# Kernel tuning notes

Hardware: AMD Instinct MI355X
Metric: run time of the kernel (lower is better)

Reference implementation:

```python
import jax, jax.numpy as jnp
import numpy as np
import math

DIM = 1536; NH = 12; HD = 128
F, H, W = 6, 30, 30
S = F * H * W
B = 1
K_LEN = 9900  # hardcoded k_lens in the source forward
EPS_NORM = 1e-6


def _rope_tables(max_len=1024, d=HD):
    # Wan rope_params: three tables of widths d-4*(d//6), 2*(d//6), 2*(d//6)
    # -> cos/sin tables of half-widths 22, 21, 21 (concat = d//2 = 64)
    def ang(dd):
        inv = 1.0 / (10000.0 ** (np.arange(0, dd, 2, dtype=np.float64) / dd))
        return np.outer(np.arange(max_len, dtype=np.float64), inv)
    a = np.concatenate([ang(d - 4 * (d // 6)), ang(2 * (d // 6)), ang(2 * (d // 6))], axis=1)
    return np.cos(a).astype(np.float32), np.sin(a).astype(np.float32)


def setup_inputs() -> dict:
    key = jax.random.key(0)
    ks = jax.random.split(key, 5)
    s = 1.0 / math.sqrt(DIM)
    cos, sin = _rope_tables()
    return {
        "x": jax.random.normal(ks[0], (B, S, DIM), jnp.float32),
        "q_w": jax.random.normal(ks[1], (DIM, DIM), jnp.float32) * s,
        "q_b": jnp.zeros((DIM,), jnp.float32),
        "k_w": jax.random.normal(ks[2], (DIM, DIM), jnp.float32) * s,
        "k_b": jnp.zeros((DIM,), jnp.float32),
        "v_w": jax.random.normal(ks[3], (DIM, DIM), jnp.float32) * s,
        "v_b": jnp.zeros((DIM,), jnp.float32),
        "o_w": jax.random.normal(ks[4], (DIM, DIM), jnp.float32) * s,
        "o_b": jnp.zeros((DIM,), jnp.float32),
        "norm_q_w": jnp.ones((DIM,), jnp.float32),
        "norm_k_w": jnp.ones((DIM,), jnp.float32),
        "freqs_cos": jnp.asarray(cos),
        "freqs_sin": jnp.asarray(sin),
        "grid_f": F, "grid_h": H, "grid_w": W,
    }


def rms_norm(x, w):
    # RMSNorm over full model dim, computed in fp32 (as in source)
    xf = x.astype(jnp.float32)
    xn = xf * jax.lax.rsqrt(jnp.mean(xf * xf, axis=-1, keepdims=True) + EPS_NORM)
    return xn.astype(x.dtype) * w


def rope_apply(x, cos, sin, f, h, w):
    # x: [B,S,N,D]; rotate consecutive pairs with 3D-factorized (f,h,w) freqs
    Bb, Ss, Nn, Dd = x.shape
    c = Dd // 2
    sp = [c - 2 * (c // 3), c // 3, c // 3]  # 22, 21, 21

    def grid(tab):
        tf = tab[:, :sp[0]]
        th = tab[:, sp[0]:sp[0] + sp[1]]
        tw = tab[:, sp[0] + sp[1]:]
        g = jnp.concatenate([
            jnp.broadcast_to(tf[:f, None, None, :], (f, h, w, sp[0])),
            jnp.broadcast_to(th[None, :h, None, :], (f, h, w, sp[1])),
            jnp.broadcast_to(tw[None, None, :w, :], (f, h, w, sp[2])),
        ], axis=-1)
        return g.reshape(f * h * w, 1, c)  # [S,1,c] (broadcast over heads)

    gc, gs = grid(cos), grid(sin)
    xp = x.astype(jnp.float32).reshape(Bb, Ss, Nn, c, 2)
    xr, xi = xp[..., 0], xp[..., 1]
    orr = xr * gc - xi * gs
    oii = xr * gs + xi * gc
    return jnp.stack([orr, oii], axis=-1).reshape(Bb, Ss, Nn, Dd).astype(x.dtype)


def attention(q, k, v, k_len):
    # full attention (window_size=(-1,-1)) with keys masked beyond k_len
    scale = 1.0 / math.sqrt(q.shape[-1])
    att = jnp.einsum('bqnd,bknd->bnqk', q, k) * scale
    valid = jnp.arange(k.shape[1]) < k_len
    att = jnp.where(valid[None, None, None, :], att, jnp.finfo(att.dtype).min)
    p = jax.nn.softmax(att, axis=-1)
    return jnp.einsum('bnqk,bknd->bqnd', p, v)


def reference(x, q_w, q_b, k_w, k_b, v_w, v_b, o_w, o_b, norm_q_w, norm_k_w, freqs_cos, freqs_sin, grid_f, grid_h, grid_w):
    Bb, Ss, _ = x.shape
    q = rms_norm(x @ q_w.T + q_b, norm_q_w).reshape(Bb, Ss, NH, HD)
    k = rms_norm(x @ k_w.T + k_b, norm_k_w).reshape(Bb, Ss, NH, HD)
    v = (x @ v_w.T + v_b).reshape(Bb, Ss, NH, HD)
    q = rope_apply(q, freqs_cos, freqs_sin, grid_f, grid_h, grid_w)
    k = rope_apply(k, freqs_cos, freqs_sin, grid_f, grid_h, grid_w)
    o = attention(q, k, v, K_LEN).reshape(Bb, Ss, NH * HD)
    return o @ o_w.T + o_b
```

## Files before the change

### kernel.cpp

```cpp
#include <hip/hip_runtime.h>

#define DIM 1536
#define NH 12
#define HD 128
#define S_LEN 5400
#define SPAD 5440
#define MPAD 5504
#define NQKV 4608
#define EPS_NORM 1e-6f

typedef __bf16 bf16_t;
typedef __bf16 bf16x8 __attribute__((ext_vector_type(8)));
typedef __bf16 bf16x4 __attribute__((ext_vector_type(4)));
typedef __bf16 bf16x2 __attribute__((ext_vector_type(2)));
typedef float  f32x4  __attribute__((ext_vector_type(4)));
typedef float  f32x16 __attribute__((ext_vector_type(16)));
typedef int    i32x2  __attribute__((ext_vector_type(2)));

#define GLOAD_LDS16(gp, lp) __builtin_amdgcn_global_load_lds( \
    (__attribute__((address_space(1))) void*)(void*)(gp),     \
    (__attribute__((address_space(3))) void*)(lp), 16, 0, 0)

__device__ __forceinline__ unsigned int pkbf(float a, float b) {
  union { bf16x2 h; unsigned int u; } c;
  c.h[0] = (__bf16)a; c.h[1] = (__bf16)b;
  return c.u;
}

__device__ __forceinline__ float xhalf_max(float x) {
  i32x2 r = __builtin_amdgcn_permlane32_swap(__float_as_int(x), __float_as_int(x),
                                             false, false);
  return fmaxf(__int_as_float(r.x), __int_as_float(r.y));
}
__device__ __forceinline__ float xhalf_sum(float x) {
  i32x2 r = __builtin_amdgcn_permlane32_swap(__float_as_int(x), __float_as_int(x),
                                             false, false);
  return __int_as_float(r.x) + __int_as_float(r.y);
}


__global__ __launch_bounds__(256) void cvt_x_kernel(const float* __restrict__ x,
                                                    bf16_t* __restrict__ xb) {
  size_t base = ((size_t)blockIdx.x * 256 + threadIdx.x) * 4;
  if (base >= (size_t)MPAD * DIM) return;
  size_t row = base / DIM;
  float4 v = make_float4(0.f, 0.f, 0.f, 0.f);
  if (row < S_LEN) v = *(const float4*)&x[base];
  bf16x4 o; o[0] = (__bf16)v.x; o[1] = (__bf16)v.y; o[2] = (__bf16)v.z; o[3] = (__bf16)v.w;
  *(bf16x4*)&xb[base] = o;
}

__global__ __launch_bounds__(256) void cvt_wqkv_kernel(const float* __restrict__ qw,
                                                       const float* __restrict__ kw,
                                                       const float* __restrict__ vw,
                                                       bf16_t* __restrict__ wb) {
  size_t base = ((size_t)blockIdx.x * 256 + threadIdx.x) * 4;
  if (base >= (size_t)NQKV * DIM) return;
  int row = (int)(base / DIM);
  int col = (int)(base - (size_t)row * DIM);
  const float* src; int rr = row;
  if (rr >= 3072)      { src = vw; rr -= 3072; }
  else if (rr >= 1536) { src = kw; rr -= 1536; }
  else                 { src = qw; }
  float4 v = *(const float4*)&src[(size_t)rr * DIM + col];
  bf16x4 o; o[0] = (__bf16)v.x; o[1] = (__bf16)v.y; o[2] = (__bf16)v.z; o[3] = (__bf16)v.w;
  *(bf16x4*)&wb[base] = o;
}

__global__ __launch_bounds__(256) void cvt_wo_kernel(const float* __restrict__ w,
                                                     bf16_t* __restrict__ wb) {
  size_t base = ((size_t)blockIdx.x * 256 + threadIdx.x) * 4;
  if (base >= (size_t)DIM * DIM) return;
  float4 v = *(const float4*)&w[base];
  bf16x4 o; o[0] = (__bf16)v.x; o[1] = (__bf16)v.y; o[2] = (__bf16)v.z; o[3] = (__bf16)v.w;
  *(bf16x4*)&wb[base] = o;
}


template<bool OUT_BF16>
__global__ __launch_bounds__(256) void gemm_bt_kernel(
    const bf16_t* __restrict__ A, const bf16_t* __restrict__ B, void* __restrict__ C,
    const float* __restrict__ bias0, const float* __restrict__ bias1,
    const float* __restrict__ bias2, int M, int N, int K, int Mvalid) {
  __shared__ bf16_t As[2][128 * 32];
  __shared__ bf16_t Bs[2][128 * 32];
  int tid = threadIdx.x;
  int lane = tid & 63, wave = tid >> 6, quad = lane >> 4, l16 = lane & 15;
  int m0 = blockIdx.y * 128, n0 = blockIdx.x * 128;
  int wm = (wave >> 1) * 64, wn = (wave & 1) * 64;
  const bf16_t* Ab = A + (size_t)m0 * K;
  const bf16_t* Bb = B + (size_t)n0 * K;
  f32x4 acc[4][4] = {};

  int eo0 = tid * 8;
  int row0 = eo0 >> 5, col0 = eo0 & 31;
  int eo1 = (256 + tid) * 8;
  int row1 = eo1 >> 5, col1 = eo1 & 31;

  GLOAD_LDS16(Ab + (size_t)row0 * K + col0, &As[0][eo0]);
  GLOAD_LDS16(Bb + (size_t)row0 * K + col0, &Bs[0][eo0]);
  GLOAD_LDS16(Ab + (size_t)row1 * K + col1, &As[0][eo1]);
  GLOAD_LDS16(Bb + (size_t)row1 * K + col1, &Bs[0][eo1]);
  asm volatile("s_waitcnt vmcnt(0)" ::: "memory");
  __builtin_amdgcn_s_barrier();
  __builtin_amdgcn_sched_barrier(0);

  int KT = K >> 5;
  for (int t = 0; t < KT; t++) {
    int cur = t & 1;
    if (t + 1 < KT) {
      int kn = (t + 1) << 5;
      GLOAD_LDS16(Ab + (size_t)row0 * K + kn + col0, &As[cur ^ 1][eo0]);
      GLOAD_LDS16(Bb + (size_t)row0 * K + kn + col0, &Bs[cur ^ 1][eo0]);
      GLOAD_LDS16(Ab + (size_t)row1 * K + kn + col1, &As[cur ^ 1][eo1]);
      GLOAD_LDS16(Bb + (size_t)row1 * K + kn + col1, &Bs[cur ^ 1][eo1]);
    }
    bf16x8 af[4], bfr[4];
#pragma unroll
    for (int i = 0; i < 4; i++)
      af[i] = *(const bf16x8*)&As[cur][(wm + i * 16 + l16) * 32 + quad * 8];
#pragma unroll
    for (int j = 0; j < 4; j++)
      bfr[j] = *(const bf16x8*)&Bs[cur][(wn + j * 16 + l16) * 32 + quad * 8];
#pragma unroll
    for (int i = 0; i < 4; i++)
#pragma unroll
      for (int j = 0; j < 4; j++)
        acc[i][j] = __builtin_amdgcn_mfma_f32_16x16x32_bf16(af[i], bfr[j], acc[i][j], 0, 0, 0);
    asm volatile("s_waitcnt vmcnt(0) lgkmcnt(0)" ::: "memory");
    __builtin_amdgcn_s_barrier();
    __builtin_amdgcn_sched_barrier(0);
  }
#pragma unroll
  for (int j = 0; j < 4; j++) {
    int n = n0 + wn + j * 16 + l16;
    float bias = (n < 1536) ? bias0[n] : (n < 3072) ? bias1[n - 1536] : bias2[n - 3072];
#pragma unroll
    for (int i = 0; i < 4; i++) {
#pragma unroll
      for (int r = 0; r < 4; r++) {
        int m = m0 + wm + i * 16 + quad * 4 + r;
        float v = acc[i][j][r] + bias;
        if (OUT_BF16) {
          ((bf16_t*)C)[(size_t)m * N + n] = (__bf16)v;
        } else {
          if (m < Mvalid) ((float*)C)[(size_t)m * N + n] = v;
        }
      }
    }
  }
}


__global__ __launch_bounds__(256) void rope_qk_kernel(
    const bf16_t* __restrict__ qkv, const float* __restrict__ nqw,
    const float* __restrict__ nkw, const float* __restrict__ fcos,
    const float* __restrict__ fsin, bf16_t* __restrict__ qout,
    bf16_t* __restrict__ kout) {
  int s = blockIdx.x;
  int tid = threadIdx.x;
  bool valid = s < S_LEN;
  int f = s / 900, hh = (s / 30) % 30, ww = s % 30;
  __shared__ float red[4];
  for (int which = 0; which < 2; which++) {
    const bf16_t* src = qkv + (size_t)s * NQKV + which * DIM;
    const float* nw = which ? nkw : nqw;
    bf16_t* dst = (which ? kout : qout) + (size_t)s * DIM;
    float osc = which ? 1.0f : 0.12751742686f;
    float v[6]; float ss = 0.f;
#pragma unroll
    for (int i = 0; i < 6; i++) {
      v[i] = valid ? (float)src[tid * 6 + i] : 0.f;
      ss += v[i] * v[i];
    }
#pragma unroll
    for (int off = 32; off >= 1; off >>= 1) ss += __shfl_down(ss, off);
    if ((tid & 63) == 0) red[tid >> 6] = ss;
    __syncthreads();
    float tot = red[0] + red[1] + red[2] + red[3];
    float rn = rsqrtf(tot * (1.f / DIM) + EPS_NORM);
    __syncthreads();
#pragma unroll
    for (int i = 0; i < 3; i++) {
      int e0 = tid * 6 + 2 * i;
      int p = e0 >> 1;
      int cc = p & 63;
      int pos = (cc < 22) ? f : (cc < 43) ? hh : ww;
      float c = fcos[pos * 64 + cc], sn = fsin[pos * 64 + cc];
      float xr = v[2 * i] * rn * nw[e0];
      float xi = v[2 * i + 1] * rn * nw[e0 + 1];
      dst[e0]     = (__bf16)((xr * c - xi * sn) * osc);
      dst[e0 + 1] = (__bf16)((xr * sn + xi * c) * osc);
    }
  }
}


__global__ __launch_bounds__(256) void v_transpose_kernel(const bf16_t* __restrict__ qkv,
                                                          bf16_t* __restrict__ vt) {
  __shared__ bf16_t tile[64][136];
  int h = blockIdx.y, s0 = blockIdx.x * 64, tid = threadIdx.x;
#pragma unroll
  for (int it = 0; it < 4; it++) {
    int eo = (it * 256 + tid) * 8;
    int row = eo >> 7, col = eo & 127;
    int s = s0 + row;
    bf16x8 val = {};
    if (s < S_LEN) val = *(const bf16x8*)&qkv[(size_t)s * NQKV + 3072 + h * HD + col];
    *(bf16x8*)&tile[row][col] = val;
  }
  __syncthreads();
  int d = tid & 127, j0 = (tid >> 7) * 32;
  bf16x8 outv[4];
#pragma unroll
  for (int b = 0; b < 4; b++)
#pragma unroll
    for (int j = 0; j < 8; j++) outv[b][j] = tile[j0 + b * 8 + j][d];
  size_t base = ((size_t)h * HD + d) * SPAD + s0 + j0;
#pragma unroll
  for (int b = 0; b < 4; b++) *(bf16x8*)&vt[base + b * 8] = outv[b];
}


__global__ __launch_bounds__(256, 2) void flash_attn_kernel(
    const bf16_t* __restrict__ q, const bf16_t* __restrict__ k,
    const bf16_t* __restrict__ vt, bf16_t* __restrict__ o) {
  __shared__ bf16_t Ks[2][64 * 128];
  __shared__ bf16_t Vs[2][64 * 128];
  int head = blockIdx.y;
  int s0 = blockIdx.x * 128;
  int tid = threadIdx.x, w = tid >> 6, lane = tid & 63;
  int l31 = lane & 31, hh = lane >> 5;

  bf16x8 bq[8];
  {
    const bf16_t* qp = &q[(size_t)(s0 + w * 32 + l31) * DIM + head * HD + hh * 8];
#pragma unroll
    for (int kc = 0; kc < 8; kc++) bq[kc] = *(const bf16x8*)(qp + kc * 16);
  }

  float m_i = -1e30f, l_i = 0.f;
  f32x16 oacc[4] = {};

  const int NT = SPAD / 64;

#pragma unroll
  for (int it = 0; it < 4; it++) {
    int slot = it * 256 + tid;
    int row = slot >> 4, pc = slot & 15;
    int c = pc ^ (row & 15);
    GLOAD_LDS16(k + (size_t)row * DIM + head * HD + c * 8, &Ks[0][slot * 8]);
  }
#pragma unroll
  for (int it = 0; it < 4; it++) {
    int slot = it * 256 + tid;
    int row = slot >> 4, pc = slot & 15;
    int cp = pc ^ (row & 15);
    int d = 2 * row + (cp >> 3);
    GLOAD_LDS16(vt + ((size_t)head * HD + d) * SPAD + (cp & 7) * 8, &Vs[0][slot * 8]);
  }
  asm volatile("s_waitcnt vmcnt(0)" ::: "memory");
  __builtin_amdgcn_s_barrier();
  __builtin_amdgcn_sched_barrier(0);

  for (int t = 0; t < NT; t++) {
    int kt = t * 64;
    int cur = t & 1;

    if (t + 1 < NT) {
      int kn = kt + 64;
#pragma unroll
      for (int it = 0; it < 4; it++) {
        int slot = it * 256 + tid;
        int row = slot >> 4, pc = slot & 15;
        int c = pc ^ (row & 15);
        GLOAD_LDS16(k + (size_t)(kn + row) * DIM + head * HD + c * 8, &Ks[cur ^ 1][slot * 8]);
      }
#pragma unroll
      for (int it = 0; it < 4; it++) {
        int slot = it * 256 + tid;
        int row = slot >> 4, pc = slot & 15;
        int cp = pc ^ (row & 15);
        int d = 2 * row + (cp >> 3);
        GLOAD_LDS16(vt + ((size_t)head * HD + d) * SPAD + kn + (cp & 7) * 8, &Vs[cur ^ 1][slot * 8]);
      }
    }

    f32x16 sacc[2] = {};
    __builtin_amdgcn_s_setprio(1);
#pragma unroll
    for (int ns = 0; ns < 2; ns++) {
      int row = ns * 32 + l31;
#pragma unroll
      for (int kc = 0; kc < 8; kc++) {
        int pc = (kc * 2 + hh) ^ (row & 15);
        bf16x8 ak = *(const bf16x8*)&Ks[cur][row * 128 + pc * 8];
        sacc[ns] = __builtin_amdgcn_mfma_f32_32x32x16_bf16(ak, bq[kc], sacc[ns], 0, 0, 0);
      }
    }
    __builtin_amdgcn_s_setprio(0);

    if (kt + 64 > S_LEN) {
#pragma unroll
      for (int ns = 0; ns < 2; ns++)
#pragma unroll
        for (int r = 0; r < 16; r++) {
          int kvg = kt + ns * 32 + (r & 3) + 8 * (r >> 2) + 4 * hh;
          if (kvg >= S_LEN) sacc[ns][r] = -1e30f;
        }
    }

    float mx;
    {
      float tm[8];
#pragma unroll
      for (int i = 0; i < 8; i++)
        tm[i] = fmaxf(fmaxf(sacc[0][i], sacc[0][i + 8]),
                      fmaxf(sacc[1][i], sacc[1][i + 8]));
#pragma unroll
      for (int i = 0; i < 4; i++) tm[i] = fmaxf(tm[i], tm[i + 4]);
      mx = fmaxf(fmaxf(tm[0], tm[2]), fmaxf(tm[1], tm[3]));
    }
    mx = xhalf_max(mx);
    if (!__all(mx - m_i <= 11.5f)) {
      float mn = fmaxf(m_i, mx);
      float al = __builtin_amdgcn_exp2f(m_i - mn);
      l_i *= al;
#pragma unroll
      for (int dt = 0; dt < 4; dt++)
#pragma unroll
        for (int r = 0; r < 16; r++) oacc[dt][r] *= al;
      m_i = mn;
    }
#pragma unroll
    for (int ns = 0; ns < 2; ns++)
#pragma unroll
      for (int r = 0; r < 16; r++)
        sacc[ns][r] = __builtin_amdgcn_exp2f(sacc[ns][r] - m_i);
    float rs;
    {
      float ts[8];
#pragma unroll
      for (int i = 0; i < 8; i++)
        ts[i] = (sacc[0][i] + sacc[0][i + 8]) + (sacc[1][i] + sacc[1][i + 8]);
#pragma unroll
      for (int i = 0; i < 4; i++) ts[i] += ts[i + 4];
      rs = (ts[0] + ts[2]) + (ts[1] + ts[3]);
    }
    l_i += xhalf_sum(rs);

    __builtin_amdgcn_s_setprio(1);
#pragma unroll
    for (int kvc = 0; kvc < 4; kvc++) {
      int ns = kvc >> 1, rb = (kvc & 1) * 8;
      int w0 = (int)pkbf(sacc[ns][rb + 0], sacc[ns][rb + 1]);
      int w1 = (int)pkbf(sacc[ns][rb + 2], sacc[ns][rb + 3]);
      int w2 = (int)pkbf(sacc[ns][rb + 4], sacc[ns][rb + 5]);
      int w3 = (int)pkbf(sacc[ns][rb + 6], sacc[ns][rb + 7]);
      i32x2 r02 = __builtin_amdgcn_permlane32_swap(w0, w2, false, false);
      i32x2 r13 = __builtin_amdgcn_permlane32_swap(w1, w3, false, false);
      union { unsigned int u[4]; bf16x8 v8; } bpu;
      bpu.u[0] = (unsigned int)r02.x; bpu.u[1] = (unsigned int)r13.x;
      bpu.u[2] = (unsigned int)r02.y; bpu.u[3] = (unsigned int)r13.y;
      bf16x8 bp = bpu.v8;
#pragma unroll
      for (int dt = 0; dt < 4; dt++) {
        int d = dt * 32 + l31;
        int r = d >> 1;
        int cp = ((d & 1) << 3) | (kvc * 2 + hh);
        int pc = cp ^ (r & 15);
        bf16x8 av = *(const bf16x8*)&Vs[cur][r * 128 + pc * 8];
        oacc[dt] = __builtin_amdgcn_mfma_f32_32x32x16_bf16(av, bp, oacc[dt], 0, 0, 0);
      }
    }
    __builtin_amdgcn_s_setprio(0);

    asm volatile("s_waitcnt vmcnt(0) lgkmcnt(0)" ::: "memory");
    __builtin_amdgcn_s_barrier();
    __builtin_amdgcn_sched_barrier(0);
  }

  bf16_t* scr = ((bf16_t*)Ks) + w * (32 * 64);
  float inv = 1.f / l_i;
  int qr = lane >> 1, seg = lane & 1;
  int srow = s0 + w * 32 + qr;
#pragma unroll
  for (int half = 0; half < 2; half++) {
#pragma unroll
    for (int dl = 0; dl < 2; dl++) {
      int dt = half * 2 + dl;
#pragma unroll
      for (int tt = 0; tt < 4; tt++) {
        bf16x4 v;
#pragma unroll
        for (int r4 = 0; r4 < 4; r4++) v[r4] = (__bf16)(oacc[dt][tt * 4 + r4] * inv);
        int c8 = dl * 8 + 2 * tt + hh;
        int pc8 = c8 ^ (l31 & 15);
        *(bf16x4*)&scr[l31 * 64 + pc8 * 4] = v;
      }
    }
#pragma unroll
    for (int i = 0; i < 4; i++) {
      int c8 = seg * 8 + 2 * i;
      bf16x4 lo = *(const bf16x4*)&scr[qr * 64 + ((c8) ^ (qr & 15)) * 4];
      bf16x4 hi = *(const bf16x4*)&scr[qr * 64 + ((c8 + 1) ^ (qr & 15)) * 4];
      bf16x8 val;
#pragma unroll
      for (int j = 0; j < 4; j++) { val[j] = lo[j]; val[j + 4] = hi[j]; }
      if (srow < S_LEN)
        *(bf16x8*)&o[(size_t)srow * DIM + head * HD + half * 64 + seg * 32 + i * 8] = val;
    }
  }
}


extern "C" void kernel_launch(void* const* d_in, const int* in_sizes, int n_in,
                              void* d_out, int out_size, void* d_ws, size_t ws_size,
                              hipStream_t stream) {
  const float* x    = (const float*)d_in[0];
  const float* q_w  = (const float*)d_in[1];
  const float* q_b  = (const float*)d_in[2];
  const float* k_w  = (const float*)d_in[3];
  const float* k_b  = (const float*)d_in[4];
  const float* v_w  = (const float*)d_in[5];
  const float* v_b  = (const float*)d_in[6];
  const float* o_w  = (const float*)d_in[7];
  const float* o_b  = (const float*)d_in[8];
  const float* nqw  = (const float*)d_in[9];
  const float* nkw  = (const float*)d_in[10];
  const float* fcos = (const float*)d_in[11];
  const float* fsin = (const float*)d_in[12];

  char* ws = (char*)d_ws;
  bf16_t* xb   = (bf16_t*)(ws + 0);
  bf16_t* wqkv = (bf16_t*)(ws + 16908288);
  bf16_t* wob  = (bf16_t*)(ws + 31064064);
  bf16_t* qkv  = (bf16_t*)(ws + 35782656);
  bf16_t* qb   = (bf16_t*)(ws + 86507520);
  bf16_t* kb   = (bf16_t*)(ws + 103415808);
  bf16_t* vtb  = (bf16_t*)(ws + 0);
  bf16_t* aob  = (bf16_t*)(ws + 35782656);

  cvt_x_kernel<<<(MPAD * DIM / 4 + 255) / 256, 256, 0, stream>>>(x, xb);
  cvt_wqkv_kernel<<<(NQKV * DIM / 4 + 255) / 256, 256, 0, stream>>>(q_w, k_w, v_w, wqkv);
  cvt_wo_kernel<<<(DIM * DIM / 4 + 255) / 256, 256, 0, stream>>>(o_w, wob);

  gemm_bt_kernel<true><<<dim3(NQKV / 128, MPAD / 128), 256, 0, stream>>>(
      xb, wqkv, qkv, q_b, k_b, v_b, MPAD, NQKV, DIM, MPAD);

  rope_qk_kernel<<<MPAD, 256, 0, stream>>>(qkv, nqw, nkw, fcos, fsin, qb, kb);
  v_transpose_kernel<<<dim3(SPAD / 64, NH), 256, 0, stream>>>(qkv, vtb);

  flash_attn_kernel<<<dim3(MPAD / 128, NH), 256, 0, stream>>>(qb, kb, vtb, aob);

  gemm_bt_kernel<false><<<dim3(DIM / 128, MPAD / 128), 256, 0, stream>>>(
      aob, wob, d_out, o_b, o_b, o_b, MPAD, DIM, DIM, S_LEN);
}
```

Before: 657.5 us.

## Split flash attention over two KV halves with a combine kernel

Splits the key/value sequence into two halves along a new grid dimension, so the attention launch has twice as many blocks. Each half writes unnormalized fp32 partial outputs plus running max and sum, and a new combine kernel merges them into the bf16 attention output. The double-buffered LDS prefetch is replaced by single-buffered synchronous loads, which halves LDS use and allows four blocks per CU. The cost is a load wait on every tile with no overlap, extra fp32 global traffic for the partials, and one more kernel launch.

```diff
diff --git a/kernel.cpp b/kernel.cpp
--- a/kernel.cpp
+++ b/kernel.cpp
@@ -222,12 +222,15 @@
 }
 
 
-__global__ __launch_bounds__(256, 2) void flash_attn_kernel(
+__global__ __launch_bounds__(256, 4) void flash_attn_kernel(
     const bf16_t* __restrict__ q, const bf16_t* __restrict__ k,
-    const bf16_t* __restrict__ vt, bf16_t* __restrict__ o) {
-  __shared__ bf16_t Ks[2][64 * 128];
-  __shared__ bf16_t Vs[2][64 * 128];
+    const bf16_t* __restrict__ vt, float* __restrict__ op0,
+    float* __restrict__ op1, float* __restrict__ mlp) {
+  __shared__ __align__(16) char lds_raw[32768];
+  bf16_t* Ks = (bf16_t*)lds_raw;
+  bf16_t* Vs = (bf16_t*)(lds_raw + 16384);
   int head = blockIdx.y;
+  int kvh = blockIdx.z;
   int s0 = blockIdx.x * 128;
   int tid = threadIdx.x, w = tid >> 6, lane = tid & 63;
   int l31 = lane & 31, hh = lane >> 5;
@@ -242,49 +245,30 @@
   float m_i = -1e30f, l_i = 0.f;
   f32x16 oacc[4] = {};
 
-  const int NT = SPAD / 64;
-
-#pragma unroll
-  for (int it = 0; it < 4; it++) {
-    int slot = it * 256 + tid;
-    int row = slot >> 4, pc = slot & 15;
-    int c = pc ^ (row & 15);
-    GLOAD_LDS16(k + (size_t)row * DIM + head * HD + c * 8, &Ks[0][slot * 8]);
-  }
-#pragma unroll
-  for (int it = 0; it < 4; it++) {
-    int slot = it * 256 + tid;
-    int row = slot >> 4, pc = slot & 15;
-    int cp = pc ^ (row & 15);
-    int d = 2 * row + (cp >> 3);
-    GLOAD_LDS16(vt + ((size_t)head * HD + d) * SPAD + (cp & 7) * 8, &Vs[0][slot * 8]);
-  }
-  asm volatile("s_waitcnt vmcnt(0)" ::: "memory");
-  __builtin_amdgcn_s_barrier();
-  __builtin_amdgcn_sched_barrier(0);
-
-  for (int t = 0; t < NT; t++) {
+  int tstart = kvh ? 43 : 0;
+  int tend   = kvh ? 85 : 43;
+
+  for (int t = tstart; t < tend; t++) {
     int kt = t * 64;
-    int cur = t & 1;
-
-    if (t + 1 < NT) {
-      int kn = kt + 64;
-#pragma unroll
-      for (int it = 0; it < 4; it++) {
-        int slot = it * 256 + tid;
-        int row = slot >> 4, pc = slot & 15;
-        int c = pc ^ (row & 15);
-        GLOAD_LDS16(k + (size_t)(kn + row) * DIM + head * HD + c * 8, &Ks[cur ^ 1][slot * 8]);
-      }
-#pragma unroll
-      for (int it = 0; it < 4; it++) {
-        int slot = it * 256 + tid;
-        int row = slot >> 4, pc = slot & 15;
-        int cp = pc ^ (row & 15);
-        int d = 2 * row + (cp >> 3);
-        GLOAD_LDS16(vt + ((size_t)head * HD + d) * SPAD + kn + (cp & 7) * 8, &Vs[cur ^ 1][slot * 8]);
-      }
-    }
+
+#pragma unroll
+    for (int it = 0; it < 4; it++) {
+      int slot = it * 256 + tid;
+      int row = slot >> 4, pc = slot & 15;
+      int c = pc ^ (row & 15);
+      GLOAD_LDS16(k + (size_t)(kt + row) * DIM + head * HD + c * 8, &Ks[slot * 8]);
+    }
+#pragma unroll
+    for (int it = 0; it < 4; it++) {
+      int slot = it * 256 + tid;
+      int row = slot >> 4, pc = slot & 15;
+      int cp = pc ^ (row & 15);
+      int d = 2 * row + (cp >> 3);
+      GLOAD_LDS16(vt + ((size_t)head * HD + d) * SPAD + kt + (cp & 7) * 8, &Vs[slot * 8]);
+    }
+    asm volatile("s_waitcnt vmcnt(0)" ::: "memory");
+    __builtin_amdgcn_s_barrier();
+    __builtin_amdgcn_sched_barrier(0);
 
     f32x16 sacc[2] = {};
     __builtin_amdgcn_s_setprio(1);
@@ -294,7 +278,7 @@
 #pragma unroll
       for (int kc = 0; kc < 8; kc++) {
         int pc = (kc * 2 + hh) ^ (row & 15);
-        bf16x8 ak = *(const bf16x8*)&Ks[cur][row * 128 + pc * 8];
+        bf16x8 ak = *(const bf16x8*)&Ks[row * 128 + pc * 8];
         sacc[ns] = __builtin_amdgcn_mfma_f32_32x32x16_bf16(ak, bq[kc], sacc[ns], 0, 0, 0);
       }
     }
@@ -369,48 +353,75 @@
         int r = d >> 1;
         int cp = ((d & 1) << 3) | (kvc * 2 + hh);
         int pc = cp ^ (r & 15);
-        bf16x8 av = *(const bf16x8*)&Vs[cur][r * 128 + pc * 8];
+        bf16x8 av = *(const bf16x8*)&Vs[r * 128 + pc * 8];
         oacc[dt] = __builtin_amdgcn_mfma_f32_32x32x16_bf16(av, bp, oacc[dt], 0, 0, 0);
       }
     }
     __builtin_amdgcn_s_setprio(0);
 
-    asm volatile("s_waitcnt vmcnt(0) lgkmcnt(0)" ::: "memory");
+    asm volatile("s_waitcnt lgkmcnt(0)" ::: "memory");
     __builtin_amdgcn_s_barrier();
     __builtin_amdgcn_sched_barrier(0);
   }
 
-  bf16_t* scr = ((bf16_t*)Ks) + w * (32 * 64);
-  float inv = 1.f / l_i;
+  float* scrf = (float*)(lds_raw + (size_t)w * 8192);
+  float* op = kvh ? op1 : op0;
   int qr = lane >> 1, seg = lane & 1;
   int srow = s0 + w * 32 + qr;
 #pragma unroll
-  for (int half = 0; half < 2; half++) {
+  for (int dhalf = 0; dhalf < 2; dhalf++) {
 #pragma unroll
     for (int dl = 0; dl < 2; dl++) {
-      int dt = half * 2 + dl;
+      int dt = dhalf * 2 + dl;
 #pragma unroll
       for (int tt = 0; tt < 4; tt++) {
-        bf16x4 v;
-#pragma unroll
-        for (int r4 = 0; r4 < 4; r4++) v[r4] = (__bf16)(oacc[dt][tt * 4 + r4] * inv);
+        f32x4 v;
+#pragma unroll
+        for (int r4 = 0; r4 < 4; r4++) v[r4] = oacc[dt][tt * 4 + r4];
         int c8 = dl * 8 + 2 * tt + hh;
         int pc8 = c8 ^ (l31 & 15);
-        *(bf16x4*)&scr[l31 * 64 + pc8 * 4] = v;
+        *(f32x4*)&scrf[l31 * 64 + pc8 * 4] = v;
       }
     }
 #pragma unroll
     for (int i = 0; i < 4; i++) {
       int c8 = seg * 8 + 2 * i;
-      bf16x4 lo = *(const bf16x4*)&scr[qr * 64 + ((c8) ^ (qr & 15)) * 4];
-      bf16x4 hi = *(const bf16x4*)&scr[qr * 64 + ((c8 + 1) ^ (qr & 15)) * 4];
-      bf16x8 val;
-#pragma unroll
-      for (int j = 0; j < 4; j++) { val[j] = lo[j]; val[j + 4] = hi[j]; }
-      if (srow < S_LEN)
-        *(bf16x8*)&o[(size_t)srow * DIM + head * HD + half * 64 + seg * 32 + i * 8] = val;
-    }
-  }
+      f32x4 lo = *(const f32x4*)&scrf[qr * 64 + ((c8) ^ (qr & 15)) * 4];
+      f32x4 hi = *(const f32x4*)&scrf[qr * 64 + ((c8 + 1) ^ (qr & 15)) * 4];
+      size_t ob = ((size_t)srow * NH + head) * HD + dhalf * 64 + seg * 32 + i * 8;
+      *(f32x4*)&op[ob] = lo;
+      *(f32x4*)&op[ob + 4] = hi;
+    }
+  }
+  if (hh == 0) {
+    int qg = s0 + w * 32 + l31;
+    *(float2*)&mlp[(((size_t)kvh * NH + head) * MPAD + qg) * 2] = make_float2(m_i, l_i);
+  }
+}
+
+
+__global__ __launch_bounds__(256) void combine_kernel(
+    const float* __restrict__ op0, const float* __restrict__ op1,
+    const float* __restrict__ mlp, bf16_t* __restrict__ aob) {
+  size_t idx = (size_t)blockIdx.x * 256 + threadIdx.x;
+  if (idx >= (size_t)MPAD * NH * 32) return;
+  int dc = (int)(idx & 31);
+  int head = (int)((idx >> 5) % NH);
+  int s = (int)(idx / (NH * 32));
+  float2 a0 = *(const float2*)&mlp[(((size_t)0 * NH + head) * MPAD + s) * 2];
+  float2 a1 = *(const float2*)&mlp[(((size_t)1 * NH + head) * MPAD + s) * 2];
+  float m = fmaxf(a0.x, a1.x);
+  float w0 = __builtin_amdgcn_exp2f(a0.x - m);
+  float w1 = __builtin_amdgcn_exp2f(a1.x - m);
+  float inv = 1.f / (a0.y * w0 + a1.y * w1);
+  w0 *= inv; w1 *= inv;
+  size_t ob = ((size_t)s * NH + head) * HD + (size_t)dc * 4;
+  f32x4 x0 = *(const f32x4*)&op0[ob];
+  f32x4 x1 = *(const f32x4*)&op1[ob];
+  bf16x4 o4;
+#pragma unroll
+  for (int j = 0; j < 4; j++) o4[j] = (__bf16)(x0[j] * w0 + x1[j] * w1);
+  *(bf16x4*)&aob[ob] = o4;
 }
 
 
@@ -439,7 +450,10 @@
   bf16_t* qb   = (bf16_t*)(ws + 86507520);
   bf16_t* kb   = (bf16_t*)(ws + 103415808);
   bf16_t* vtb  = (bf16_t*)(ws + 0);
-  bf16_t* aob  = (bf16_t*)(ws + 35782656);
+  float*  op0p = (float*)(ws + 35782656);
+  float*  op1p = (float*)(ws + 120324096);
+  float*  mlpp = (float*)(ws + 154140672);
+  bf16_t* aob  = (bf16_t*)(ws + 103415808);
 
   cvt_x_kernel<<<(MPAD * DIM / 4 + 255) / 256, 256, 0, stream>>>(x, xb);
   cvt_wqkv_kernel<<<(NQKV * DIM / 4 + 255) / 256, 256, 0, stream>>>(q_w, k_w, v_w, wqkv);
@@ -451,7 +465,11 @@
   rope_qk_kernel<<<MPAD, 256, 0, stream>>>(qkv, nqw, nkw, fcos, fsin, qb, kb);
   v_transpose_kernel<<<dim3(SPAD / 64, NH), 256, 0, stream>>>(qkv, vtb);
 
-  flash_attn_kernel<<<dim3(MPAD / 128, NH), 256, 0, stream>>>(qb, kb, vtb, aob);
+  flash_attn_kernel<<<dim3(MPAD / 128, NH, 2), 256, 0, stream>>>(
+      qb, kb, vtb, op0p, op1p, mlpp);
+
+  combine_kernel<<<(MPAD * NH * 32 + 255) / 256, 256, 0, stream>>>(
+      op0p, op1p, mlpp, aob);
 
   gemm_bt_kernel<false><<<dim3(DIM / 128, MPAD / 128), 256, 0, stream>>>(
       aob, wob, d_out, o_b, o_b, o_b, MPAD, DIM, DIM, S_LEN);
```

Result: slower. 1.074 ms (+63.4%).

## Use 128-key tiles without double buffering and XCD-aware block remap in flash attention

Applied to the files above, without the earlier changes.

The flash attention kernel now processes 128 keys per iteration instead of 64, halving the number of barriers and softmax rescale steps per query block. The K/V double buffer is dropped: each iteration loads the full tile, waits, then computes, so global loads no longer overlap with MFMA work. A 1D grid with an XCD-aware remap groups blocks of the same head onto one XCD to improve L2 reuse of K/V. SPAD grows to 5504 so the padded length divides by 128, which adds some masked padding work and loses load/compute overlap.

```diff
diff --git a/kernel.cpp b/kernel.cpp
--- a/kernel.cpp
+++ b/kernel.cpp
@@ -4,7 +4,7 @@
 #define NH 12
 #define HD 128
 #define S_LEN 5400
-#define SPAD 5440
+#define SPAD 5504
 #define MPAD 5504
 #define NQKV 4608
 #define EPS_NORM 1e-6f
@@ -225,10 +225,17 @@
 __global__ __launch_bounds__(256, 2) void flash_attn_kernel(
     const bf16_t* __restrict__ q, const bf16_t* __restrict__ k,
     const bf16_t* __restrict__ vt, bf16_t* __restrict__ o) {
-  __shared__ bf16_t Ks[2][64 * 128];
-  __shared__ bf16_t Vs[2][64 * 128];
-  int head = blockIdx.y;
-  int s0 = blockIdx.x * 128;
+  __shared__ __align__(16) char lds_raw[65536];
+  bf16_t* Ks = (bf16_t*)lds_raw;
+  bf16_t* Vs = (bf16_t*)(lds_raw + 32768);
+  int nwg = gridDim.x;
+  int bid = blockIdx.x;
+  int xcd = bid & 7, idx = bid >> 3;
+  int q8 = nwg >> 3, rr = nwg & 7;
+  int work = (xcd < rr ? xcd * (q8 + 1) : rr * (q8 + 1) + (xcd - rr) * q8) + idx;
+  int head = work / 43;
+  int s0 = (work - head * 43) * 128;
+
   int tid = threadIdx.x, w = tid >> 6, lane = tid & 63;
   int l31 = lane & 31, hh = lane >> 5;
 
@@ -242,67 +249,50 @@
   float m_i = -1e30f, l_i = 0.f;
   f32x16 oacc[4] = {};
 
-  const int NT = SPAD / 64;
-
-#pragma unroll
-  for (int it = 0; it < 4; it++) {
-    int slot = it * 256 + tid;
-    int row = slot >> 4, pc = slot & 15;
-    int c = pc ^ (row & 15);
-    GLOAD_LDS16(k + (size_t)row * DIM + head * HD + c * 8, &Ks[0][slot * 8]);
-  }
-#pragma unroll
-  for (int it = 0; it < 4; it++) {
-    int slot = it * 256 + tid;
-    int row = slot >> 4, pc = slot & 15;
-    int cp = pc ^ (row & 15);
-    int d = 2 * row + (cp >> 3);
-    GLOAD_LDS16(vt + ((size_t)head * HD + d) * SPAD + (cp & 7) * 8, &Vs[0][slot * 8]);
-  }
-  asm volatile("s_waitcnt vmcnt(0)" ::: "memory");
-  __builtin_amdgcn_s_barrier();
-  __builtin_amdgcn_sched_barrier(0);
+  const int NT = SPAD / 128;
 
   for (int t = 0; t < NT; t++) {
-    int kt = t * 64;
-    int cur = t & 1;
-
-    if (t + 1 < NT) {
-      int kn = kt + 64;
-#pragma unroll
-      for (int it = 0; it < 4; it++) {
-        int slot = it * 256 + tid;
-        int row = slot >> 4, pc = slot & 15;
-        int c = pc ^ (row & 15);
-        GLOAD_LDS16(k + (size_t)(kn + row) * DIM + head * HD + c * 8, &Ks[cur ^ 1][slot * 8]);
-      }
+    int kt = t * 128;
+
+#pragma unroll
+    for (int it = 0; it < 8; it++) {
+      int slot = it * 256 + tid;
+      int row = slot >> 4, pc = slot & 15;
+      int c = pc ^ (row & 15);
+      GLOAD_LDS16(k + (size_t)(kt + row) * DIM + head * HD + c * 8, &Ks[slot * 8]);
+    }
+#pragma unroll
+    for (int h2 = 0; h2 < 2; h2++)
 #pragma unroll
       for (int it = 0; it < 4; it++) {
         int slot = it * 256 + tid;
         int row = slot >> 4, pc = slot & 15;
         int cp = pc ^ (row & 15);
         int d = 2 * row + (cp >> 3);
-        GLOAD_LDS16(vt + ((size_t)head * HD + d) * SPAD + kn + (cp & 7) * 8, &Vs[cur ^ 1][slot * 8]);
-      }
-    }
-
-    f32x16 sacc[2] = {};
+        GLOAD_LDS16(vt + ((size_t)head * HD + d) * SPAD + kt + h2 * 64 + (cp & 7) * 8,
+                    &Vs[h2 * 8192 + slot * 8]);
+      }
+    asm volatile("s_waitcnt vmcnt(0)" ::: "memory");
+    __builtin_amdgcn_s_barrier();
+    __builtin_amdgcn_sched_barrier(0);
+
+    f32x16 sacc[4] = {};
     __builtin_amdgcn_s_setprio(1);
 #pragma unroll
-    for (int ns = 0; ns < 2; ns++) {
+    for (int ns = 0; ns < 4; ns++) {
       int row = ns * 32 + l31;
 #pragma unroll
       for (int kc = 0; kc < 8; kc++) {
         int pc = (kc * 2 + hh) ^ (row & 15);
-        bf16x8 ak = *(const bf16x8*)&Ks[cur][row * 128 + pc * 8];
+        bf16x8 ak = *(const bf16x8*)&Ks[row * 128 + pc * 8];
         sacc[ns] = __builtin_amdgcn_mfma_f32_32x32x16_bf16(ak, bq[kc], sacc[ns], 0, 0, 0);
       }
     }
     __builtin_amdgcn_s_setprio(0);
 
-    if (kt + 64 > S_LEN) {
-#pragma unroll
-      for (int ns = 0; ns < 2; ns++)
+    if (kt + 128 > S_LEN) {
+#pragma unroll
+      for (int ns = 0; ns < 4; ns++)
 #pragma unroll
         for (int r = 0; r < 16; r++) {
           int kvg = kt + ns * 32 + (r & 3) + 8 * (r >> 2) + 4 * hh;
@@ -314,9 +304,13 @@
     {
       float tm[8];
 #pragma unroll
-      for (int i = 0; i < 8; i++)
-        tm[i] = fmaxf(fmaxf(sacc[0][i], sacc[0][i + 8]),
-                      fmaxf(sacc[1][i], sacc[1][i + 8]));
+      for (int i = 0; i < 8; i++) {
+        float a = fmaxf(fmaxf(sacc[0][i], sacc[0][i + 8]),
+                        fmaxf(sacc[1][i], sacc[1][i + 8]));
+        float b = fmaxf(fmaxf(sacc[2][i], sacc[2][i + 8]),
+                        fmaxf(sacc[3][i], sacc[3][i + 8]));
+        tm[i] = fmaxf(a, b);
+      }
 #pragma unroll
       for (int i = 0; i < 4; i++) tm[i] = fmaxf(tm[i], tm[i + 4]);
       mx = fmaxf(fmaxf(tm[0], tm[2]), fmaxf(tm[1], tm[3]));
@@ -333,7 +327,7 @@
       m_i = mn;
     }
 #pragma unroll
-    for (int ns = 0; ns < 2; ns++)
+    for (int ns = 0; ns < 4; ns++)
 #pragma unroll
       for (int r = 0; r < 16; r++)
         sacc[ns][r] = __builtin_amdgcn_exp2f(sacc[ns][r] - m_i);
@@ -342,7 +336,8 @@
       float ts[8];
 #pragma unroll
       for (int i = 0; i < 8; i++)
-        ts[i] = (sacc[0][i] + sacc[0][i + 8]) + (sacc[1][i] + sacc[1][i + 8]);
+        ts[i] = ((sacc[0][i] + sacc[0][i + 8]) + (sacc[1][i] + sacc[1][i + 8])) +
+                ((sacc[2][i] + sacc[2][i + 8]) + (sacc[3][i] + sacc[3][i + 8]));
 #pragma unroll
       for (int i = 0; i < 4; i++) ts[i] += ts[i + 4];
       rs = (ts[0] + ts[2]) + (ts[1] + ts[3]);
@@ -351,7 +346,7 @@
 
     __builtin_amdgcn_s_setprio(1);
 #pragma unroll
-    for (int kvc = 0; kvc < 4; kvc++) {
+    for (int kvc = 0; kvc < 8; kvc++) {
       int ns = kvc >> 1, rb = (kvc & 1) * 8;
       int w0 = (int)pkbf(sacc[ns][rb + 0], sacc[ns][rb + 1]);
       int w1 = (int)pkbf(sacc[ns][rb + 2], sacc[ns][rb + 3]);
@@ -363,24 +358,26 @@
       bpu.u[0] = (unsigned int)r02.x; bpu.u[1] = (unsigned int)r13.x;
       bpu.u[2] = (unsigned int)r02.y; bpu.u[3] = (unsigned int)r13.y;
       bf16x8 bp = bpu.v8;
+      int h2 = kvc >> 2, kvl = kvc & 3;
+      const bf16_t* Vh = Vs + h2 * 8192;
 #pragma unroll
       for (int dt = 0; dt < 4; dt++) {
         int d = dt * 32 + l31;
         int r = d >> 1;
-        int cp = ((d & 1) << 3) | (kvc * 2 + hh);
+        int cp = ((d & 1) << 3) | (kvl * 2 + hh);
         int pc = cp ^ (r & 15);
-        bf16x8 av = *(const bf16x8*)&Vs[cur][r * 128 + pc * 8];
+        bf16x8 av = *(const bf16x8*)&Vh[r * 128 + pc * 8];
         oacc[dt] = __builtin_amdgcn_mfma_f32_32x32x16_bf16(av, bp, oacc[dt], 0, 0, 0);
       }
     }
     __builtin_amdgcn_s_setprio(0);
 
-    asm volatile("s_waitcnt vmcnt(0) lgkmcnt(0)" ::: "memory");
+    asm volatile("s_waitcnt lgkmcnt(0)" ::: "memory");
     __builtin_amdgcn_s_barrier();
     __builtin_amdgcn_sched_barrier(0);
   }
 
-  bf16_t* scr = ((bf16_t*)Ks) + w * (32 * 64);
+  bf16_t* scr = Ks + w * (32 * 64);
   float inv = 1.f / l_i;
   int qr = lane >> 1, seg = lane & 1;
   int srow = s0 + w * 32 + qr;
@@ -451,7 +448,7 @@
   rope_qk_kernel<<<MPAD, 256, 0, stream>>>(qkv, nqw, nkw, fcos, fsin, qb, kb);
   v_transpose_kernel<<<dim3(SPAD / 64, NH), 256, 0, stream>>>(qkv, vtb);
 
-  flash_attn_kernel<<<dim3(MPAD / 128, NH), 256, 0, stream>>>(qb, kb, vtb, aob);
+  flash_attn_kernel<<<dim3((MPAD / 128) * NH), 256, 0, stream>>>(qb, kb, vtb, aob);
 
   gemm_bt_kernel<false><<<dim3(DIM / 128, MPAD / 128), 256, 0, stream>>>(
       aob, wob, d_out, o_b, o_b, o_b, MPAD, DIM, DIM, S_LEN);
```

After: 657.1 us. No clear change (-0.1%).

## Replace QKV projection GEMM with 256x256-tile 512-thread pipelined kernel

Applied to the files above, without the earlier changes.

Adds a dedicated QKV GEMM kernel that uses 256x256 output tiles, 8 waves, and a 64-wide K step. A/B tiles are double-buffered in LDS through direct global-to-LDS loads with an XOR swizzle, and next-stage loads are interleaved across four compute phases with explicit waitcnt and priority control. The goal is higher arithmetic intensity and better overlap of memory and MFMA than the 128x128 generic kernel. In exchange, M is padded to 5632 rows (more wasted work), the workspace offsets shift, and LDS use is large (128KB per block).

```diff
diff --git a/kernel.cpp b/kernel.cpp
--- a/kernel.cpp
+++ b/kernel.cpp
@@ -6,6 +6,7 @@
 #define S_LEN 5400
 #define SPAD 5440
 #define MPAD 5504
+#define MPAD2 5632
 #define NQKV 4608
 #define EPS_NORM 1e-6f
 
@@ -42,7 +43,7 @@
 __global__ __launch_bounds__(256) void cvt_x_kernel(const float* __restrict__ x,
                                                     bf16_t* __restrict__ xb) {
   size_t base = ((size_t)blockIdx.x * 256 + threadIdx.x) * 4;
-  if (base >= (size_t)MPAD * DIM) return;
+  if (base >= (size_t)MPAD2 * DIM) return;
   size_t row = base / DIM;
   float4 v = make_float4(0.f, 0.f, 0.f, 0.f);
   if (row < S_LEN) v = *(const float4*)&x[base];
@@ -74,6 +75,106 @@
   float4 v = *(const float4*)&w[base];
   bf16x4 o; o[0] = (__bf16)v.x; o[1] = (__bf16)v.y; o[2] = (__bf16)v.z; o[3] = (__bf16)v.w;
   *(bf16x4*)&wb[base] = o;
+}
+
+
+__global__ __launch_bounds__(512, 2) void gemm1_256_kernel(
+    const bf16_t* __restrict__ A, const bf16_t* __restrict__ B,
+    bf16_t* __restrict__ C, const float* __restrict__ bias0,
+    const float* __restrict__ bias1, const float* __restrict__ bias2) {
+  const int K = 1536, N = NQKV, KT = 24;
+  __shared__ bf16_t lds[2][2][256 * 64];
+  int tid = threadIdx.x;
+  int lane = tid & 63, wave = tid >> 6, quad = lane >> 4, l16 = lane & 15;
+  int wm2 = wave >> 2, wn4 = wave & 3;
+  int m0 = blockIdx.y * 256, n0 = blockIdx.x * 256;
+  const bf16_t* Ab = A + (size_t)m0 * K;
+  const bf16_t* Bb = B + (size_t)n0 * K;
+  f32x4 acc[8][4] = {};
+
+  int srow = tid >> 3, spc = tid & 7;
+  int ldst = srow * 64 + spc * 8;
+  int sc8 = (spc ^ (srow & 7)) * 8;
+
+#define G1_STAGE(buf, op, q, kt) \
+  GLOAD_LDS16((op ? Bb : Ab) + (size_t)((q) * 64 + srow) * K + (kt) + sc8, \
+              &lds[buf][op][(q) * 64 * 64 + ldst])
+
+  G1_STAGE(0, 1, 0, 0); G1_STAGE(0, 1, 1, 0);
+  G1_STAGE(0, 1, 2, 0); G1_STAGE(0, 1, 3, 0);
+  G1_STAGE(0, 0, 0, 0); G1_STAGE(0, 0, 2, 0);
+  G1_STAGE(0, 0, 1, 0); G1_STAGE(0, 0, 3, 0);
+
+  int pcq0 = (0 * 4 + quad) ^ (l16 & 7);
+  int pcq1 = (1 * 4 + quad) ^ (l16 & 7);
+
+  for (int t = 0; t < KT; t++) {
+    int cur = t & 1, nxt = cur ^ 1;
+    int kn = (t + 1) * 64;
+    bool st = (t + 1 < KT);
+
+#define G1_PHASE(mh, nh2, STAGES, WAITS)                                      \
+    {                                                                         \
+      WAITS;                                                                  \
+      __builtin_amdgcn_s_barrier();                                           \
+      __builtin_amdgcn_sched_barrier(0);                                      \
+      bf16x8 af[4][2], bfv[2][2];                                             \
+      _Pragma("unroll")                                                       \
+      for (int i2 = 0; i2 < 4; i2++) {                                        \
+        int row = wm2 * 128 + ((mh) * 4 + i2) * 16 + l16;                     \
+        af[i2][0] = *(const bf16x8*)&lds[cur][0][row * 64 + pcq0 * 8];        \
+        af[i2][1] = *(const bf16x8*)&lds[cur][0][row * 64 + pcq1 * 8];        \
+      }                                                                       \
+      _Pragma("unroll")                                                       \
+      for (int j2 = 0; j2 < 2; j2++) {                                        \
+        int rowb = wn4 * 64 + ((nh2) * 2 + j2) * 16 + l16;                    \
+        bfv[j2][0] = *(const bf16x8*)&lds[cur][1][rowb * 64 + pcq0 * 8];      \
+        bfv[j2][1] = *(const bf16x8*)&lds[cur][1][rowb * 64 + pcq1 * 8];      \
+      }                                                                       \
+      if (st) { STAGES; }                                                     \
+      asm volatile("s_waitcnt lgkmcnt(0)" ::: "memory");                      \
+      __builtin_amdgcn_sched_barrier(0);                                      \
+      __builtin_amdgcn_s_setprio(1);                                          \
+      _Pragma("unroll")                                                       \
+      for (int i2 = 0; i2 < 4; i2++)                                          \
+        _Pragma("unroll")                                                     \
+        for (int j2 = 0; j2 < 2; j2++)                                        \
+          _Pragma("unroll")                                                   \
+          for (int kk = 0; kk < 2; kk++)                                      \
+            acc[(mh) * 4 + i2][(nh2) * 2 + j2] =                              \
+                __builtin_amdgcn_mfma_f32_16x16x32_bf16(                      \
+                    af[i2][kk], bfv[j2][kk],                                  \
+                    acc[(mh) * 4 + i2][(nh2) * 2 + j2], 0, 0, 0);             \
+      __builtin_amdgcn_s_setprio(0);                                          \
+    }
+
+    G1_PHASE(0, 0, G1_STAGE(nxt,1,0,kn); G1_STAGE(nxt,1,1,kn),
+             if (st) asm volatile("s_waitcnt vmcnt(2)" ::: "memory");
+             else    asm volatile("s_waitcnt vmcnt(0)" ::: "memory"));
+    G1_PHASE(1, 0, G1_STAGE(nxt,1,2,kn); G1_STAGE(nxt,1,3,kn),
+             if (st) asm volatile("s_waitcnt vmcnt(2)" ::: "memory");
+             else    asm volatile("s_waitcnt vmcnt(0)" ::: "memory"));
+    G1_PHASE(0, 1, G1_STAGE(nxt,0,0,kn); G1_STAGE(nxt,0,2,kn),
+             asm volatile("s_waitcnt vmcnt(4)" ::: "memory"));
+    G1_PHASE(1, 1, G1_STAGE(nxt,0,1,kn); G1_STAGE(nxt,0,3,kn),
+             asm volatile("s_waitcnt vmcnt(6)" ::: "memory"));
+#undef G1_PHASE
+  }
+#undef G1_STAGE
+
+#pragma unroll
+  for (int j = 0; j < 4; j++) {
+    int n = n0 + wn4 * 64 + j * 16 + l16;
+    float bias = (n < 1536) ? bias0[n] : (n < 3072) ? bias1[n - 1536] : bias2[n - 3072];
+#pragma unroll
+    for (int i = 0; i < 8; i++) {
+#pragma unroll
+      for (int r = 0; r < 4; r++) {
+        int m = m0 + wm2 * 128 + i * 16 + quad * 4 + r;
+        C[(size_t)m * N + n] = (__bf16)(acc[i][j][r] + bias);
+      }
+    }
+  }
 }
 
 
@@ -433,20 +534,20 @@
 
   char* ws = (char*)d_ws;
   bf16_t* xb   = (bf16_t*)(ws + 0);
-  bf16_t* wqkv = (bf16_t*)(ws + 16908288);
-  bf16_t* wob  = (bf16_t*)(ws + 31064064);
-  bf16_t* qkv  = (bf16_t*)(ws + 35782656);
-  bf16_t* qb   = (bf16_t*)(ws + 86507520);
-  bf16_t* kb   = (bf16_t*)(ws + 103415808);
+  bf16_t* wqkv = (bf16_t*)(ws + 17301504);
+  bf16_t* wob  = (bf16_t*)(ws + 31457280);
+  bf16_t* qkv  = (bf16_t*)(ws + 36175872);
+  bf16_t* qb   = (bf16_t*)(ws + 88080384);
+  bf16_t* kb   = (bf16_t*)(ws + 104988672);
   bf16_t* vtb  = (bf16_t*)(ws + 0);
-  bf16_t* aob  = (bf16_t*)(ws + 35782656);
-
-  cvt_x_kernel<<<(MPAD * DIM / 4 + 255) / 256, 256, 0, stream>>>(x, xb);
+  bf16_t* aob  = (bf16_t*)(ws + 36175872);
+
+  cvt_x_kernel<<<(MPAD2 * DIM / 4 + 255) / 256, 256, 0, stream>>>(x, xb);
   cvt_wqkv_kernel<<<(NQKV * DIM / 4 + 255) / 256, 256, 0, stream>>>(q_w, k_w, v_w, wqkv);
   cvt_wo_kernel<<<(DIM * DIM / 4 + 255) / 256, 256, 0, stream>>>(o_w, wob);
 
-  gemm_bt_kernel<true><<<dim3(NQKV / 128, MPAD / 128), 256, 0, stream>>>(
-      xb, wqkv, qkv, q_b, k_b, v_b, MPAD, NQKV, DIM, MPAD);
+  gemm1_256_kernel<<<dim3(NQKV / 256, MPAD2 / 256), 512, 0, stream>>>(
+      xb, wqkv, qkv, q_b, k_b, v_b);
 
   rope_qk_kernel<<<MPAD, 256, 0, stream>>>(qkv, nqw, nkw, fcos, fsin, qb, kb);
   v_transpose_kernel<<<dim3(SPAD / 64, NH), 256, 0, stream>>>(qkv, vtb);
```

Result: faster. 643.8 us (-2.1%).
